# Kernel optimization log

Measured on AMD Instinct MI355X. Metric: run time of the kernel, lower is better.

The kernel has to match this reference:

```python
import jax, jax.numpy as jnp
import numpy as np

N, E, G, DIN, DH = 50000, 800000, 256, 128, 128
BN_EPS = 1e-5


def _gin_layer(h, src, dst, W1, b1, gamma, beta, W2, b2):
    # GINConv (eps=0): agg_i = sum_{(j->i) in edges} h_j ; z = agg + h
    agg = jnp.zeros_like(h).at[dst].add(h[src])
    z = agg + h
    z = z @ W1 + b1
    # BatchNorm1d (training mode: batch stats over nodes, biased var)
    mean = z.mean(axis=0)
    var = z.var(axis=0)
    z = gamma * (z - mean) * jax.lax.rsqrt(var + BN_EPS) + beta
    z = jax.nn.relu(z)
    z = z @ W2 + b2
    return jax.nn.relu(z)


def setup_inputs() -> dict:
    key = jax.random.key(0)
    ks = jax.random.split(key, 12)
    x = jax.random.normal(ks[0], (N, DIN), dtype=jnp.float32)
    edge_index = jax.random.randint(ks[1], (2, E), 0, N, dtype=jnp.int32)
    batch = jnp.sort(jax.random.randint(ks[2], (N,), 0, G, dtype=jnp.int32))
    s = 0.05
    W1 = jax.random.normal(ks[3], (7, DIN, DH), dtype=jnp.float32) * s
    b1 = jnp.zeros((7, DH), dtype=jnp.float32)
    gamma = jnp.ones((7, DH), dtype=jnp.float32)
    beta = jnp.zeros((7, DH), dtype=jnp.float32)
    W2 = jax.random.normal(ks[4], (7, DH, DH), dtype=jnp.float32) * s
    b2 = jnp.zeros((7, DH), dtype=jnp.float32)
    Wl1 = jax.random.normal(ks[5], (14 * DH, 14 * DH), dtype=jnp.float32) * s
    bl1 = jnp.zeros((14 * DH,), dtype=jnp.float32)
    Wl2 = jax.random.normal(ks[6], (14 * DH, 1), dtype=jnp.float32) * s
    bl2 = jnp.zeros((1,), dtype=jnp.float32)
    return {"x": x, "edge_index": edge_index, "batch": batch,
            "W1": W1, "b1": b1, "gamma": gamma, "beta": beta,
            "W2": W2, "b2": b2, "Wl1": Wl1, "bl1": bl1,
            "Wl2": Wl2, "bl2": bl2}


def reference(x, edge_index, batch, W1, b1, gamma, beta, W2, b2, Wl1, bl1, Wl2, bl2):
    src, dst = edge_index[0], edge_index[1]
    hs = []
    h = x
    for i in range(7):
        h = _gin_layer(h, src, dst, W1[i], b1[i], gamma[i], beta[i], W2[i], b2[i])
        hs.append(h)
    adds = [jax.ops.segment_sum(hi, batch, num_segments=G) for hi in hs]
    maxs = [jax.ops.segment_max(hi, batch, num_segments=G) for hi in hs]
    h = jnp.concatenate(adds + maxs, axis=1)  # [G, 14*DH]
    h = jax.nn.relu(h @ Wl1 + bl1)
    h = h @ Wl2 + bl2
    return (jax.nn.sigmoid(h), h)
```

## Files before the change

kernel.cpp:

```cpp
#include <hip/hip_runtime.h>
#include <cstdint>
#include <cstddef>

#define NN 50000
#define NE 800000
#define NG 256
#define NLAY 7
#define NBLK 782
#define NBLK1 1563
#define CAP 18432

typedef float f32x4 __attribute__((ext_vector_type(4)));
typedef __bf16 bf16x8 __attribute__((ext_vector_type(8)));
typedef _Float16 h16x8 __attribute__((ext_vector_type(8)));

__device__ __forceinline__ float4 ld4(const float* p) { return *(const float4*)p; }
__device__ __forceinline__ void addh8(float4& x, float4& y, h16x8 v) {
  x.x += (float)v[0]; x.y += (float)v[1]; x.z += (float)v[2]; x.w += (float)v[3];
  y.x += (float)v[4]; y.y += (float)v[5]; y.z += (float)v[6]; y.w += (float)v[7];
}

__global__ void k_init(const float* __restrict__ x, const float* __restrict__ W1,
                       const float* __restrict__ W2, int* __restrict__ counts,
                       int* __restrict__ gcur, float* __restrict__ pooled,
                       _Float16* __restrict__ hb,
                       __bf16* __restrict__ w1f, __bf16* __restrict__ w2f) {
  int i = blockIdx.x * 256 + threadIdx.x;
  if (i < NN) counts[i] = 0;
  if (i < 49) gcur[i] = i * CAP;
  if (i < NG * 1792) pooled[i] = 0.f;
  if (i < NN * 128) hb[i] = (_Float16)x[i];
  if (i < NLAY * 32768) {
    int l = i >> 15, pos = i & 32767;
    int j = pos & 7, ln = (pos >> 3) & 63, slot = (pos >> 9) & 15, kc = pos >> 13;
    int hl = slot & 1, ctp = (slot >> 1) & 3, hfp = slot >> 3;
    int n = hfp * 64 + ctp * 16 + (ln & 15);
    int k = kc * 32 + ((ln >> 4) << 3) + j;
    float a = W1[l * 16384 + k * 128 + n];
    float b = W2[l * 16384 + k * 128 + n];
    __bf16 ah = (__bf16)a, bh = (__bf16)b;
    w1f[i] = hl ? (__bf16)(a - (float)ah) : ah;
    w2f[i] = hl ? (__bf16)(b - (float)bh) : bh;
  }
}

__global__ void k_hist(const int* __restrict__ edge, int* __restrict__ counts) {
  int e = blockIdx.x * 256 + threadIdx.x;
  if (e < NE) atomicAdd(&counts[edge[NE + e]], 1);
}

__global__ void k_part(const int* __restrict__ counts, int* __restrict__ bsum) {
  __shared__ int sm[256];
  int b = blockIdx.x, t = threadIdx.x;
  int i = b * 256 + t;
  sm[t] = (i < NN) ? counts[i] : 0;
  __syncthreads();
  for (int s = 128; s > 0; s >>= 1) {
    if (t < s) sm[t] += sm[t + s];
    __syncthreads();
  }
  if (t == 0) bsum[b] = sm[0];
}

__global__ void k_bscan(const int* __restrict__ bsum, int* __restrict__ boff,
                        int* __restrict__ row_ptr) {
  __shared__ int sm[256];
  int t = threadIdx.x;
  int v = (t < 196) ? bsum[t] : 0;
  sm[t] = v;
  __syncthreads();
  int val = v;
  for (int off = 1; off < 256; off <<= 1) {
    int o = (t >= off) ? sm[t - off] : 0;
    __syncthreads();
    val += o;
    sm[t] = val;
    __syncthreads();
  }
  if (t < 196) boff[t] = val - v;
  if (t == 255) row_ptr[NN] = val;
}

__global__ void k_rowptr(const int* __restrict__ counts, const int* __restrict__ boff,
                         int* __restrict__ row_ptr) {
  __shared__ int sm[256];
  int b = blockIdx.x, t = threadIdx.x;
  int i = b * 256 + t;
  int c = (i < NN) ? counts[i] : 0;
  sm[t] = c;
  __syncthreads();
  int val = c;
  for (int off = 1; off < 256; off <<= 1) {
    int o = (t >= off) ? sm[t - off] : 0;
    __syncthreads();
    val += o;
    sm[t] = val;
    __syncthreads();
  }
  if (i < NN) row_ptr[i] = val - c + boff[b];
}

__global__ __launch_bounds__(256) void k_binA(const int* __restrict__ edge,
                                              int* __restrict__ gcur,
                                              unsigned int* __restrict__ bins) {
  __shared__ int lh[49], lbase[49], lt[49];
  const int tid = threadIdx.x;
  const int e0 = blockIdx.x * 3125, e1 = e0 + 3125;
  if (tid < 49) { lh[tid] = 0; lt[tid] = 0; }
  __syncthreads();
  for (int e = e0 + tid; e < e1; e += 256)
    atomicAdd(&lh[edge[NE + e] >> 10], 1);
  __syncthreads();
  if (tid < 49) lbase[tid] = atomicAdd(&gcur[tid], lh[tid]);
  __syncthreads();
  for (int e = e0 + tid; e < e1; e += 256) {
    int dst = edge[NE + e], src = edge[e];
    int r = dst >> 10;
    int t = atomicAdd(&lt[r], 1);
    bins[lbase[r] + t] = ((unsigned)dst << 16) | (unsigned)src;
  }
}

__global__ __launch_bounds__(512) void k_binB(const int* __restrict__ row_ptr,
                                              const int* __restrict__ gcur,
                                              const unsigned int* __restrict__ bins,
                                              unsigned short* __restrict__ csr16) {
  __shared__ int lcur[1024];
  __shared__ unsigned short lcsr[24576];
  const int blk = blockIdx.x, tid = threadIdx.x;
  const int base = blk << 10;
  const int nn = (base + 1024 <= NN) ? 1024 : (NN - base);
  const int seg0 = row_ptr[base];
  const int seg1 = row_ptr[(base + 1024 <= NN) ? (base + 1024) : NN];
  for (int i = tid; i < nn; i += 512) lcur[i] = row_ptr[base + i] - seg0;
  __syncthreads();
  const int tot = gcur[blk] - blk * CAP;
  for (int t = tid; t < tot; t += 512) {
    unsigned int p = bins[blk * CAP + t];
    int dst = (int)(p >> 16), src = (int)(p & 0xffffu);
    int pos = atomicAdd(&lcur[dst - base], 1);
    lcsr[pos] = (unsigned short)src;
  }
  __syncthreads();
  for (int i = tid; i < seg1 - seg0; i += 512) csr16[seg0 + i] = lcsr[i];
}

__device__ __forceinline__ void split8(const float4 v0, const float4 v1,
                                       bf16x8& hi, bf16x8& lo) {
  float f[8] = {v0.x, v0.y, v0.z, v0.w, v1.x, v1.y, v1.z, v1.w};
  #pragma unroll
  for (int j = 0; j < 8; ++j) {
    __bf16 h = (__bf16)f[j];
    hi[j] = h;
    lo[j] = (__bf16)(f[j] - (float)h);
  }
}

__device__ __forceinline__ void mfma_phase(
    int tid, const __bf16* __restrict__ wf, float (*zs)[132], f32x4 acc[4])
{
  const int wv = tid >> 6, stripe = wv >> 1, half = wv & 1;
  const int lane = tid & 63, q = lane >> 4, m = lane & 15;
  #pragma unroll
  for (int kc = 0; kc < 4; ++kc) {
    const int k0 = kc * 32 + q * 8;
    float4 v0 = *(const float4*)&zs[stripe * 16 + m][k0];
    float4 v1 = *(const float4*)&zs[stripe * 16 + m][k0 + 4];
    bf16x8 ah, al;
    split8(v0, v1, ah, al);
    #pragma unroll
    for (int ct = 0; ct < 4; ++ct) {
      const int sbase = (half * 4 + ct) * 2;
      const __bf16* bp = wf + (((size_t)(kc * 16 + sbase) * 64 + lane) << 3);
      bf16x8 bh = *(const bf16x8*)bp;
      bf16x8 bl = *(const bf16x8*)(bp + 512);
      acc[ct] = __builtin_amdgcn_mfma_f32_16x16x32_bf16(ah, bh, acc[ct], 0, 0, 0);
      acc[ct] = __builtin_amdgcn_mfma_f32_16x16x32_bf16(ah, bl, acc[ct], 0, 0, 0);
      acc[ct] = __builtin_amdgcn_mfma_f32_16x16x32_bf16(al, bh, acc[ct], 0, 0, 0);
    }
  }
  __syncthreads();
}

__global__ __launch_bounds__(512, 8) void k_fused1(
    const _Float16* __restrict__ hb, const int* __restrict__ row_ptr,
    const unsigned short* __restrict__ csr_src, const __bf16* __restrict__ wf,
    const float* __restrict__ bias, _Float16* __restrict__ zb,
    float* __restrict__ psum, float* __restrict__ psq)
{
  __shared__ float zs[32][132];
  const int tid = threadIdx.x;
  const int m0 = blockIdx.x * 32;

  {
    const int lr = tid >> 4;
    const int sub = tid & 15;
    const int r = m0 + lr;
    const int c0 = sub << 3;
    float4 a0 = make_float4(0.f, 0.f, 0.f, 0.f), a1 = a0;
    if (r < NN) {
      addh8(a0, a1, *(const h16x8*)(hb + ((size_t)r << 7) + c0));
      int e = row_ptr[r], e1 = row_ptr[r + 1];
      for (; e + 7 < e1; e += 8) {
        const h16x8 v0 = *(const h16x8*)(hb + ((size_t)csr_src[e + 0] << 7) + c0);
        const h16x8 v1 = *(const h16x8*)(hb + ((size_t)csr_src[e + 1] << 7) + c0);
        const h16x8 v2 = *(const h16x8*)(hb + ((size_t)csr_src[e + 2] << 7) + c0);
        const h16x8 v3 = *(const h16x8*)(hb + ((size_t)csr_src[e + 3] << 7) + c0);
        const h16x8 v4 = *(const h16x8*)(hb + ((size_t)csr_src[e + 4] << 7) + c0);
        const h16x8 v5 = *(const h16x8*)(hb + ((size_t)csr_src[e + 5] << 7) + c0);
        const h16x8 v6 = *(const h16x8*)(hb + ((size_t)csr_src[e + 6] << 7) + c0);
        const h16x8 v7 = *(const h16x8*)(hb + ((size_t)csr_src[e + 7] << 7) + c0);
        h16x8 t0 = v0 + v1, t1 = v2 + v3, t2 = v4 + v5, t3 = v6 + v7;
        h16x8 u0 = t0 + t1, u1 = t2 + t3;
        addh8(a0, a1, u0 + u1);
      }
      for (; e < e1; ++e)
        addh8(a0, a1, *(const h16x8*)(hb + ((size_t)csr_src[e] << 7) + c0));
    }
    *(float4*)&zs[lr][c0 + 0] = a0;
    *(float4*)&zs[lr][c0 + 4] = a1;
  }
  __syncthreads();

  const int wv = tid >> 6;
  const int stripe = wv >> 2, half = (wv >> 1) & 1, cpair = wv & 1;
  const int lane = tid & 63, q = lane >> 4, m = lane & 15;
  f32x4 acc[2] = {};
  #pragma unroll
  for (int kc = 0; kc < 4; ++kc) {
    const int k0 = kc * 32 + q * 8;
    float4 v0 = *(const float4*)&zs[stripe * 16 + m][k0];
    float4 v1 = *(const float4*)&zs[stripe * 16 + m][k0 + 4];
    bf16x8 ah, al;
    split8(v0, v1, ah, al);
    #pragma unroll
    for (int j = 0; j < 2; ++j) {
      const int ct = cpair * 2 + j;
      const int sbase = (half * 4 + ct) * 2;
      const __bf16* bp = wf + (((size_t)(kc * 16 + sbase) * 64 + lane) << 3);
      bf16x8 bh = *(const bf16x8*)bp;
      bf16x8 bl = *(const bf16x8*)(bp + 512);
      acc[j] = __builtin_amdgcn_mfma_f32_16x16x32_bf16(ah, bh, acc[j], 0, 0, 0);
      acc[j] = __builtin_amdgcn_mfma_f32_16x16x32_bf16(ah, bl, acc[j], 0, 0, 0);
      acc[j] = __builtin_amdgcn_mfma_f32_16x16x32_bf16(al, bh, acc[j], 0, 0, 0);
    }
  }
  __syncthreads();

  float* red_s = (float*)zs;
  float* red_q = red_s + 1152;
  const int sl = stripe * 4 + q;
  #pragma unroll
  for (int j = 0; j < 2; ++j) {
    const int ct = cpair * 2 + j;
    const int col = half * 64 + ct * 16 + m;
    const float bb = bias[col];
    float s = 0.f, qq = 0.f;
    #pragma unroll
    for (int i = 0; i < 4; ++i) {
      int r = m0 + stripe * 16 + q * 4 + i;
      if (r < NN) {
        float o = acc[j][i] + bb;
        zb[((size_t)r << 7) + col] = (_Float16)o;
        s += o; qq += o * o;
      }
    }
    red_s[col * 9 + sl] = s;
    red_q[col * 9 + sl] = qq;
  }
  __syncthreads();
  if (tid < 128) {
    float s = 0.f, qq = 0.f;
    #pragma unroll
    for (int k = 0; k < 8; ++k) {
      s += red_s[tid * 9 + k];
      qq += red_q[tid * 9 + k];
    }
    psum[blockIdx.x * 128 + tid] = s;
    psq[blockIdx.x * 128 + tid] = qq;
  }
}

__global__ __launch_bounds__(256) void k_bnfin(
    const float* __restrict__ psum, const float* __restrict__ psq,
    const float* __restrict__ gamma, const float* __restrict__ beta,
    float* __restrict__ ab) {
  __shared__ float ss[256], sq[256];
  int col = blockIdx.x;
  int t = threadIdx.x;
  float s = 0.f, q = 0.f;
  for (int b = t; b < NBLK1; b += 256) {
    s += psum[b * 128 + col];
    q += psq[b * 128 + col];
  }
  ss[t] = s; sq[t] = q;
  __syncthreads();
  for (int st = 128; st > 0; st >>= 1) {
    if (t < st) { ss[t] += ss[t + st]; sq[t] += sq[t + st]; }
    __syncthreads();
  }
  if (t == 0) {
    float mean = ss[0] * (1.f / NN);
    float var = sq[0] * (1.f / NN) - mean * mean;
    float rstd = rsqrtf(var + 1e-5f);
    float a = gamma[col] * rstd;
    ab[col] = a;
    ab[128 + col] = beta[col] - mean * a;
  }
}

__global__ __launch_bounds__(512) void k_fused2(
    const _Float16* __restrict__ zb, const float* __restrict__ ab,
    const __bf16* __restrict__ wf, const float* __restrict__ bias,
    _Float16* __restrict__ hb, const int* __restrict__ batch,
    float* __restrict__ pooled, int layer)
{
  __shared__ float zs[64][132];
  const int tid = threadIdx.x;
  const int m0 = blockIdx.x * 64;

  {
    const int lr = tid >> 3;
    const int sub = tid & 7;
    const int r = m0 + lr;
    const int c0 = sub << 4;
    h16x8 u0 = {}, u1 = {};
    if (r < NN) {
      const _Float16* rp = zb + ((size_t)r << 7) + c0;
      u0 = *(const h16x8*)rp;
      u1 = *(const h16x8*)(rp + 8);
    }
    float4 v0 = make_float4((float)u0[0], (float)u0[1], (float)u0[2], (float)u0[3]);
    float4 v1 = make_float4((float)u0[4], (float)u0[5], (float)u0[6], (float)u0[7]);
    float4 v2 = make_float4((float)u1[0], (float)u1[1], (float)u1[2], (float)u1[3]);
    float4 v3 = make_float4((float)u1[4], (float)u1[5], (float)u1[6], (float)u1[7]);
    float4 s0 = ld4(ab + c0), s1 = ld4(ab + c0 + 4);
    float4 s2 = ld4(ab + c0 + 8), s3 = ld4(ab + c0 + 12);
    float4 o0 = ld4(ab + 128 + c0), o1 = ld4(ab + 128 + c0 + 4);
    float4 o2 = ld4(ab + 128 + c0 + 8), o3 = ld4(ab + 128 + c0 + 12);
    float4 y0, y1, y2, y3;
    y0.x = fmaxf(fmaf(s0.x, v0.x, o0.x), 0.f); y0.y = fmaxf(fmaf(s0.y, v0.y, o0.y), 0.f);
    y0.z = fmaxf(fmaf(s0.z, v0.z, o0.z), 0.f); y0.w = fmaxf(fmaf(s0.w, v0.w, o0.w), 0.f);
    y1.x = fmaxf(fmaf(s1.x, v1.x, o1.x), 0.f); y1.y = fmaxf(fmaf(s1.y, v1.y, o1.y), 0.f);
    y1.z = fmaxf(fmaf(s1.z, v1.z, o1.z), 0.f); y1.w = fmaxf(fmaf(s1.w, v1.w, o1.w), 0.f);
    y2.x = fmaxf(fmaf(s2.x, v2.x, o2.x), 0.f); y2.y = fmaxf(fmaf(s2.y, v2.y, o2.y), 0.f);
    y2.z = fmaxf(fmaf(s2.z, v2.z, o2.z), 0.f); y2.w = fmaxf(fmaf(s2.w, v2.w, o2.w), 0.f);
    y3.x = fmaxf(fmaf(s3.x, v3.x, o3.x), 0.f); y3.y = fmaxf(fmaf(s3.y, v3.y, o3.y), 0.f);
    y3.z = fmaxf(fmaf(s3.z, v3.z, o3.z), 0.f); y3.w = fmaxf(fmaf(s3.w, v3.w, o3.w), 0.f);
    *(float4*)&zs[lr][c0 + 0] = y0;
    *(float4*)&zs[lr][c0 + 4] = y1;
    *(float4*)&zs[lr][c0 + 8] = y2;
    *(float4*)&zs[lr][c0 + 12] = y3;
  }
  __syncthreads();

  const int wv = tid >> 6, stripe = wv >> 1, half = wv & 1;
  const int lane = tid & 63, q = lane >> 4, m = lane & 15;
  f32x4 acc[4] = {};
  mfma_phase(tid, wf, zs, acc);

  int bg[4];
  #pragma unroll
  for (int i = 0; i < 4; ++i) {
    int r = m0 + stripe * 16 + q * 4 + i;
    bg[i] = (r < NN) ? batch[r] : -1;
  }
  #pragma unroll
  for (int ct = 0; ct < 4; ++ct) {
    const int col = half * 64 + ct * 16 + m;
    const float bb = bias[col];
    #pragma unroll
    for (int i = 0; i < 4; ++i) {
      int r = m0 + stripe * 16 + q * 4 + i;
      float v = fmaxf(acc[ct][i] + bb, 0.f);
      acc[ct][i] = v;
      if (r < NN) hb[((size_t)r << 7) + col] = (_Float16)v;
    }
  }

  int gstart = batch[m0];
  int gend = batch[(m0 + 63 < NN) ? (m0 + 63) : (NN - 1)];
  float* red_s = (float*)zs;
  float* red_m = red_s + 2176;
  const int sl = stripe * 4 + q;
  for (int g = gstart; g <= gend; ++g) {
    __syncthreads();
    #pragma unroll
    for (int ct = 0; ct < 4; ++ct) {
      const int col = half * 64 + ct * 16 + m;
      float s = 0.f, mx = 0.f;
      #pragma unroll
      for (int i = 0; i < 4; ++i) {
        if (bg[i] == g) { s += acc[ct][i]; mx = fmaxf(mx, acc[ct][i]); }
      }
      red_s[col * 17 + sl] = s;
      red_m[col * 17 + sl] = mx;
    }
    __syncthreads();
    if (tid < 128) {
      float s = 0.f, mx = 0.f;
      #pragma unroll
      for (int k = 0; k < 16; ++k) {
        s += red_s[tid * 17 + k];
        mx = fmaxf(mx, red_m[tid * 17 + k]);
      }
      if (s != 0.f) atomicAdd(&pooled[g * 1792 + layer * 128 + tid], s);
      if (mx != 0.f)
        atomicMax((int*)&pooled[g * 1792 + 896 + layer * 128 + tid], __float_as_int(mx));
    }
  }
}

__global__ __launch_bounds__(256) void k_wl1prep(
    const float* __restrict__ Wl1, __bf16* __restrict__ wh, __bf16* __restrict__ wl) {
  __shared__ float tile[32][33];
  const int k0 = blockIdx.x * 32, n0 = blockIdx.y * 32;
  const int lr = threadIdx.x >> 5, lc = threadIdx.x & 31;
  #pragma unroll
  for (int it = 0; it < 4; ++it) {
    int rr = lr + it * 8;
    tile[rr][lc] = Wl1[(size_t)(k0 + rr) * 1792 + n0 + lc];
  }
  __syncthreads();
  #pragma unroll
  for (int it = 0; it < 4; ++it) {
    int rr = lr + it * 8;
    float v = tile[lc][rr];
    __bf16 h = (__bf16)v;
    wh[(size_t)(n0 + rr) * 1792 + k0 + lc] = h;
    wl[(size_t)(n0 + rr) * 1792 + k0 + lc] = (__bf16)(v - (float)h);
  }
}

__global__ __launch_bounds__(256) void k_mlp1a(
    const float* __restrict__ P, const __bf16* __restrict__ wh,
    const __bf16* __restrict__ wl, float* __restrict__ part)
{
  const int tid = threadIdx.x;
  const int n0 = blockIdx.x * 64;
  const int m0 = blockIdx.y * 64;
  const int kc = blockIdx.z;
  const int kbase = kc * 448;
  const int w = tid >> 6, lane = tid & 63, q = lane >> 4, m = lane & 15;
  const int row = m0 + w * 16 + m;
  f32x4 acc[4] = {};
  const float* rp = P + (size_t)row * 1792;
  #pragma unroll 2
  for (int ks = 0; ks < 14; ++ks) {
    const int k0 = kbase + ks * 32 + q * 8;
    float4 v0 = ld4(rp + k0), v1 = ld4(rp + k0 + 4);
    bf16x8 ah, al;
    split8(v0, v1, ah, al);
    #pragma unroll
    for (int ct = 0; ct < 4; ++ct) {
      const int n = n0 + ct * 16 + m;
      bf16x8 bh = *(const bf16x8*)(wh + (size_t)n * 1792 + k0);
      bf16x8 bl = *(const bf16x8*)(wl + (size_t)n * 1792 + k0);
      acc[ct] = __builtin_amdgcn_mfma_f32_16x16x32_bf16(ah, bh, acc[ct], 0, 0, 0);
      acc[ct] = __builtin_amdgcn_mfma_f32_16x16x32_bf16(ah, bl, acc[ct], 0, 0, 0);
      acc[ct] = __builtin_amdgcn_mfma_f32_16x16x32_bf16(al, bh, acc[ct], 0, 0, 0);
    }
  }
  float* pp = part + (size_t)kc * 458752;
  #pragma unroll
  for (int ct = 0; ct < 4; ++ct) {
    const int n = n0 + ct * 16 + m;
    #pragma unroll
    for (int i = 0; i < 4; ++i) {
      int r = m0 + w * 16 + q * 4 + i;
      pp[(size_t)r * 1792 + n] = acc[ct][i];
    }
  }
}

__global__ void k_mlp2(const float* __restrict__ part, const float* __restrict__ bl1,
                       const float* __restrict__ Wl2, const float* __restrict__ bl2,
                       float* __restrict__ out) {
  __shared__ float red[256];
  int g = blockIdx.x, t = threadIdx.x;
  float p = 0.f;
  for (int k = t; k < 1792; k += 256) {
    size_t idx = (size_t)g * 1792 + k;
    float s = bl1[k];
    #pragma unroll
    for (int kc = 0; kc < 4; ++kc) s += part[(size_t)kc * 458752 + idx];
    p += fmaxf(s, 0.f) * Wl2[k];
  }
  red[t] = p;
  __syncthreads();
  for (int s = 128; s > 0; s >>= 1) {
    if (t < s) red[t] += red[t + s];
    __syncthreads();
  }
  if (t == 0) {
    float l = red[0] + bl2[0];
    out[g] = 1.f / (1.f + expf(-l));
    out[NG + g] = l;
  }
}

extern "C" void kernel_launch(void* const* d_in, const int* in_sizes, int n_in,
                              void* d_out, int out_size, void* d_ws, size_t ws_size,
                              hipStream_t stream) {
  const float* x     = (const float*)d_in[0];
  const int*   edge  = (const int*)d_in[1];
  const int*   batch = (const int*)d_in[2];
  const float* W1    = (const float*)d_in[3];
  const float* b1    = (const float*)d_in[4];
  const float* gamma = (const float*)d_in[5];
  const float* beta  = (const float*)d_in[6];
  const float* W2    = (const float*)d_in[7];
  const float* b2    = (const float*)d_in[8];
  const float* Wl1   = (const float*)d_in[9];
  const float* bl1   = (const float*)d_in[10];
  const float* Wl2   = (const float*)d_in[11];
  const float* bl2   = (const float*)d_in[12];
  float* out = (float*)d_out;

  int* wsi = (int*)d_ws;
  int* row_ptr = wsi;
  int* counts  = wsi + 50048;
  int* bsum    = wsi + 100096;
  int* boff    = wsi + 100352;
  int* gcur    = wsi + 100608;
  unsigned short* csr16 = (unsigned short*)(wsi + 100864);
  float* wsf   = (float*)(wsi + 950912);
  _Float16* zb     = (_Float16*)wsf;
  _Float16* hb     = (_Float16*)(wsf + 6400000);
  float*    part   = wsf + 9600000;
  float*    psum   = wsf + 9600000;
  float*    psq    = wsf + 9800192;
  float*    ab     = wsf + 13000192;
  float*    pooled = wsf + 13000448;
  __bf16*   w1f    = (__bf16*)(wsf + 13459200);
  __bf16*   w2f    = (__bf16*)(wsf + 13573888);
  unsigned int* bins = (unsigned int*)wsf;
  __bf16*   wl1h   = (__bf16*)wsf;
  __bf16*   wl1l   = (__bf16*)(wsf + 1605632);

  k_init<<<25000, 256, 0, stream>>>(x, W1, W2, counts, gcur, pooled, hb, w1f, w2f);
  k_hist<<<3125, 256, 0, stream>>>(edge, counts);
  k_part<<<196, 256, 0, stream>>>(counts, bsum);
  k_bscan<<<1, 256, 0, stream>>>(bsum, boff, row_ptr);
  k_rowptr<<<196, 256, 0, stream>>>(counts, boff, row_ptr);
  k_binA<<<256, 256, 0, stream>>>(edge, gcur, bins);
  k_binB<<<49, 512, 0, stream>>>(row_ptr, gcur, bins, csr16);

  for (int i = 0; i < NLAY; ++i) {
    k_fused1<<<NBLK1, 512, 0, stream>>>(hb, row_ptr, csr16, w1f + i * 32768,
                                        b1 + i * 128, zb, psum, psq);
    k_bnfin<<<128, 256, 0, stream>>>(psum, psq, gamma + i * 128, beta + i * 128, ab);
    k_fused2<<<NBLK, 512, 0, stream>>>(zb, ab, w2f + i * 32768,
                                       b2 + i * 128, hb, batch, pooled, i);
  }
  k_wl1prep<<<dim3(56, 56), 256, 0, stream>>>(Wl1, wl1h, wl1l);
  k_mlp1a<<<dim3(28, 4, 4), 256, 0, stream>>>(pooled, wl1h, wl1l, part);
  k_mlp2<<<256, 256, 0, stream>>>(part, bl1, Wl2, bl2, out);
}
```

Measured before the change: 683.1 us.

## Replace BN finalize kernel with atomic partial sums and in-kernel stat computation

Removes the separate k_bnfin kernel per layer. Each k_fused1 block now atomically adds its column sums and sums of squares into a per-layer buffer, zeroed in k_init. k_fused2 then computes the mean, rstd and scale/shift for each column into shared memory at block start. The edge-gather tail loop is also unrolled into 4/2/1 chunks. This saves seven kernel launches and the partial-buffer round trip, at the cost of atomic contention (1563 blocks x 256 atomics per layer) and nondeterministic float summation order.

```diff
diff --git a/kernel.cpp b/kernel.cpp
--- a/kernel.cpp
+++ b/kernel.cpp
@@ -24,10 +24,12 @@
                        const float* __restrict__ W2, int* __restrict__ counts,
                        int* __restrict__ gcur, float* __restrict__ pooled,
                        _Float16* __restrict__ hb,
-                       __bf16* __restrict__ w1f, __bf16* __restrict__ w2f) {
+                       __bf16* __restrict__ w1f, __bf16* __restrict__ w2f,
+                       float* __restrict__ psums) {
   int i = blockIdx.x * 256 + threadIdx.x;
   if (i < NN) counts[i] = 0;
   if (i < 49) gcur[i] = i * CAP;
+  if (i < NLAY * 256) psums[i] = 0.f;
   if (i < NG * 1792) pooled[i] = 0.f;
   if (i < NN * 128) hb[i] = (_Float16)x[i];
   if (i < NLAY * 32768) {
@@ -186,7 +188,7 @@
     const _Float16* __restrict__ hb, const int* __restrict__ row_ptr,
     const unsigned short* __restrict__ csr_src, const __bf16* __restrict__ wf,
     const float* __restrict__ bias, _Float16* __restrict__ zb,
-    float* __restrict__ psum, float* __restrict__ psq)
+    float* __restrict__ ps)
 {
   __shared__ float zs[32][132];
   const int tid = threadIdx.x;
@@ -214,7 +216,22 @@
         h16x8 u0 = t0 + t1, u1 = t2 + t3;
         addh8(a0, a1, u0 + u1);
       }
-      for (; e < e1; ++e)
+      if (e + 3 < e1) {
+        const h16x8 v0 = *(const h16x8*)(hb + ((size_t)csr_src[e + 0] << 7) + c0);
+        const h16x8 v1 = *(const h16x8*)(hb + ((size_t)csr_src[e + 1] << 7) + c0);
+        const h16x8 v2 = *(const h16x8*)(hb + ((size_t)csr_src[e + 2] << 7) + c0);
+        const h16x8 v3 = *(const h16x8*)(hb + ((size_t)csr_src[e + 3] << 7) + c0);
+        h16x8 t0 = v0 + v1, t1 = v2 + v3;
+        addh8(a0, a1, t0 + t1);
+        e += 4;
+      }
+      if (e + 1 < e1) {
+        const h16x8 v0 = *(const h16x8*)(hb + ((size_t)csr_src[e + 0] << 7) + c0);
+        const h16x8 v1 = *(const h16x8*)(hb + ((size_t)csr_src[e + 1] << 7) + c0);
+        addh8(a0, a1, v0 + v1);
+        e += 2;
+      }
+      if (e < e1)
         addh8(a0, a1, *(const h16x8*)(hb + ((size_t)csr_src[e] << 7) + c0));
     }
     *(float4*)&zs[lr][c0 + 0] = a0;
@@ -276,48 +293,33 @@
       s += red_s[tid * 9 + k];
       qq += red_q[tid * 9 + k];
     }
-    psum[blockIdx.x * 128 + tid] = s;
-    psq[blockIdx.x * 128 + tid] = qq;
-  }
-}
-
-__global__ __launch_bounds__(256) void k_bnfin(
-    const float* __restrict__ psum, const float* __restrict__ psq,
+    atomicAdd(&ps[tid], s);
+    atomicAdd(&ps[128 + tid], qq);
+  }
+}
+
+__global__ __launch_bounds__(512) void k_fused2(
+    const _Float16* __restrict__ zb, const float* __restrict__ ps,
     const float* __restrict__ gamma, const float* __restrict__ beta,
-    float* __restrict__ ab) {
-  __shared__ float ss[256], sq[256];
-  int col = blockIdx.x;
-  int t = threadIdx.x;
-  float s = 0.f, q = 0.f;
-  for (int b = t; b < NBLK1; b += 256) {
-    s += psum[b * 128 + col];
-    q += psq[b * 128 + col];
-  }
-  ss[t] = s; sq[t] = q;
-  __syncthreads();
-  for (int st = 128; st > 0; st >>= 1) {
-    if (t < st) { ss[t] += ss[t + st]; sq[t] += sq[t + st]; }
-    __syncthreads();
-  }
-  if (t == 0) {
-    float mean = ss[0] * (1.f / NN);
-    float var = sq[0] * (1.f / NN) - mean * mean;
-    float rstd = rsqrtf(var + 1e-5f);
-    float a = gamma[col] * rstd;
-    ab[col] = a;
-    ab[128 + col] = beta[col] - mean * a;
-  }
-}
-
-__global__ __launch_bounds__(512) void k_fused2(
-    const _Float16* __restrict__ zb, const float* __restrict__ ab,
     const __bf16* __restrict__ wf, const float* __restrict__ bias,
     _Float16* __restrict__ hb, const int* __restrict__ batch,
     float* __restrict__ pooled, int layer)
 {
   __shared__ float zs[64][132];
+  __shared__ float sab[256];
   const int tid = threadIdx.x;
   const int m0 = blockIdx.x * 64;
+
+  if (tid < 128) {
+    float s = ps[tid], q = ps[128 + tid];
+    float mean = s * (1.f / NN);
+    float var = q * (1.f / NN) - mean * mean;
+    float rstd = rsqrtf(var + 1e-5f);
+    float a = gamma[tid] * rstd;
+    sab[tid] = a;
+    sab[128 + tid] = beta[tid] - mean * a;
+  }
+  __syncthreads();
 
   {
     const int lr = tid >> 3;
@@ -334,10 +336,10 @@
     float4 v1 = make_float4((float)u0[4], (float)u0[5], (float)u0[6], (float)u0[7]);
     float4 v2 = make_float4((float)u1[0], (float)u1[1], (float)u1[2], (float)u1[3]);
     float4 v3 = make_float4((float)u1[4], (float)u1[5], (float)u1[6], (float)u1[7]);
-    float4 s0 = ld4(ab + c0), s1 = ld4(ab + c0 + 4);
-    float4 s2 = ld4(ab + c0 + 8), s3 = ld4(ab + c0 + 12);
-    float4 o0 = ld4(ab + 128 + c0), o1 = ld4(ab + 128 + c0 + 4);
-    float4 o2 = ld4(ab + 128 + c0 + 8), o3 = ld4(ab + 128 + c0 + 12);
+    float4 s0 = *(float4*)&sab[c0], s1 = *(float4*)&sab[c0 + 4];
+    float4 s2 = *(float4*)&sab[c0 + 8], s3 = *(float4*)&sab[c0 + 12];
+    float4 o0 = *(float4*)&sab[128 + c0], o1 = *(float4*)&sab[128 + c0 + 4];
+    float4 o2 = *(float4*)&sab[128 + c0 + 8], o3 = *(float4*)&sab[128 + c0 + 12];
     float4 y0, y1, y2, y3;
     y0.x = fmaxf(fmaf(s0.x, v0.x, o0.x), 0.f); y0.y = fmaxf(fmaf(s0.y, v0.y, o0.y), 0.f);
     y0.z = fmaxf(fmaf(s0.z, v0.z, o0.z), 0.f); y0.w = fmaxf(fmaf(s0.w, v0.w, o0.w), 0.f);
@@ -528,9 +530,7 @@
   _Float16* zb     = (_Float16*)wsf;
   _Float16* hb     = (_Float16*)(wsf + 6400000);
   float*    part   = wsf + 9600000;
-  float*    psum   = wsf + 9600000;
-  float*    psq    = wsf + 9800192;
-  float*    ab     = wsf + 13000192;
+  float*    psums  = wsf + 12800000;
   float*    pooled = wsf + 13000448;
   __bf16*   w1f    = (__bf16*)(wsf + 13459200);
   __bf16*   w2f    = (__bf16*)(wsf + 13573888);
@@ -538,7 +538,8 @@
   __bf16*   wl1h   = (__bf16*)wsf;
   __bf16*   wl1l   = (__bf16*)(wsf + 1605632);
 
-  k_init<<<25000, 256, 0, stream>>>(x, W1, W2, counts, gcur, pooled, hb, w1f, w2f);
+  k_init<<<25000, 256, 0, stream>>>(x, W1, W2, counts, gcur, pooled, hb, w1f, w2f,
+                                    psums);
   k_hist<<<3125, 256, 0, stream>>>(edge, counts);
   k_part<<<196, 256, 0, stream>>>(counts, bsum);
   k_bscan<<<1, 256, 0, stream>>>(bsum, boff, row_ptr);
@@ -548,9 +549,9 @@
 
   for (int i = 0; i < NLAY; ++i) {
     k_fused1<<<NBLK1, 512, 0, stream>>>(hb, row_ptr, csr16, w1f + i * 32768,
-                                        b1 + i * 128, zb, psum, psq);
-    k_bnfin<<<128, 256, 0, stream>>>(psum, psq, gamma + i * 128, beta + i * 128, ab);
-    k_fused2<<<NBLK, 512, 0, stream>>>(zb, ab, w2f + i * 32768,
+                                        b1 + i * 128, zb, psums + i * 256);
+    k_fused2<<<NBLK, 512, 0, stream>>>(zb, psums + i * 256, gamma + i * 128,
+                                       beta + i * 128, w2f + i * 32768,
                                        b2 + i * 128, hb, batch, pooled, i);
   }
   k_wl1prep<<<dim3(56, 56), 256, 0, stream>>>(Wl1, wl1h, wl1l);
```

Measured after the change: 778.4 us. 1.14x slower.
